# Kernel tuning notes

Measured on AMD Instinct MI355X. Metric: run time of the kernel, lower is better.

The kernel has to match this reference:

```python
import jax, jax.numpy as jnp
import numpy as np

N_NODES = 50000
N_EDGES = 800000
IN_CH = 64
HID = 128


def setup_inputs() -> dict:
    key = jax.random.key(0)
    ks = jax.random.split(key, 10)
    x = jax.random.normal(ks[0], (N_NODES, IN_CH), dtype=jnp.float32)
    edge_index = jax.random.randint(ks[1], (2, N_EDGES), 0, N_NODES, dtype=jnp.int64)
    def lin(k, fan_in, fan_out):
        bound = 1.0 / np.sqrt(fan_in)
        kw, kb = jax.random.split(k)
        W = jax.random.uniform(kw, (fan_in, fan_out), minval=-bound, maxval=bound, dtype=jnp.float32)
        b = jax.random.uniform(kb, (fan_out,), minval=-bound, maxval=bound, dtype=jnp.float32)
        return W, b
    W1a, b1a = lin(ks[2], 2 * IN_CH, HID)
    W1b, b1b = lin(ks[3], HID, HID)
    W2a, b2a = lin(ks[4], 2 * HID, HID)
    W2b, b2b = lin(ks[5], HID, HID)
    return {"x": x, "edge_index": edge_index,
            "W1a": W1a, "b1a": b1a, "W1b": W1b, "b1b": b1b,
            "W2a": W2a, "b2a": b2a, "W2b": W2b, "b2b": b2b}


def _edge_conv(x, src, dst, Wa, ba, Wb, bb):
    # PyG EdgeConv: message = MLP([x_i, x_j - x_i]), aggr = max at target i (dst)
    xi = x[dst]                                   # [E, C] target feats
    xj = x[src]                                   # [E, C] source feats
    m = jnp.concatenate([xi, xj - xi], axis=-1)   # [E, 2C]
    m = jax.nn.relu(m @ Wa + ba) @ Wb + bb        # [E, H]
    agg = jax.ops.segment_max(m, dst, num_segments=N_NODES)
    # nodes with no incoming edge -> 0 (torch_scatter fill value)
    return jnp.where(jnp.isfinite(agg), agg, 0.0)


def reference(x, edge_index, W1a, b1a, W1b, b1b, W2a, b2a, W2b, b2b):
    src = edge_index[0]
    dst = edge_index[1]
    h = _edge_conv(x, src, dst, W1a, b1a, W1b, b1b)
    h = jax.nn.relu(h)
    h = _edge_conv(h, src, dst, W2a, b2a, W2b, b2b)
    return h
```

## Files before the change

kernel.cpp:

```cpp
#include <hip/hip_runtime.h>
#include <stdint.h>

#define N_NODES 50000
#define N_EDGES 800000
#define HID 128
#define NWG_E (N_EDGES / 128)
#define XQ (NWG_E / 8)
#define XR (NWG_E % 8)
#define SCAN_B 196

#define ENC_NEG_INF 0x007FFFFFu

typedef short short8 __attribute__((ext_vector_type(8)));
typedef float f32x4 __attribute__((ext_vector_type(4)));

__device__ __forceinline__ unsigned enc_f32(float f) {
    unsigned u = __float_as_uint(f);
    return (u & 0x80000000u) ? ~u : (u | 0x80000000u);
}
__device__ __forceinline__ float dec_f32(unsigned e) {
    unsigned u = (e & 0x80000000u) ? (e & 0x7FFFFFFFu) : ~e;
    return __uint_as_float(u);
}
__device__ __forceinline__ unsigned short f2bf(float f) {
    unsigned u = __float_as_uint(f);
    unsigned r = (u + 0x7fffu + ((u >> 16) & 1u)) >> 16;
    return (unsigned short)r;
}
__device__ __forceinline__ float bf2f(unsigned short h) {
    return __uint_as_float(((unsigned)h) << 16);
}


__global__ void fill_u32(unsigned* __restrict__ p, int n, unsigned v) {
    int i = blockIdx.x * blockDim.x + threadIdx.x;
    int stride = gridDim.x * blockDim.x;
    for (; i < n; i += stride) p[i] = v;
}

__global__ void prep_wcat(const float* __restrict__ W, int K, float* __restrict__ WC) {
    int idx = blockIdx.x * 256 + threadIdx.x;
    if (idx >= K * 256) return;
    int k = idx >> 8, c = idx & 255;
    float v;
    if (c < 128) v = W[k * 128 + c] - W[(k + K) * 128 + c];
    else         v = W[(k + K) * 128 + (c - 128)];
    WC[idx] = v;
}

__global__ void prep_wfrag(const float* __restrict__ Wb, unsigned short* __restrict__ Wg) {
    int idx = blockIdx.x * 256 + threadIdx.x;
    int j = idx & 7, lane = (idx >> 3) & 63, nt = (idx >> 9) & 7, kt = idx >> 12;
    int k = 32 * kt + 8 * (lane >> 4) + j;
    int n = 16 * nt + (lane & 15);
    float w = Wb[k * 128 + n];
    unsigned short hi = f2bf(w);
    Wg[idx] = hi;
    Wg[16384 + idx] = f2bf(w - bf2f(hi));
}

__global__ void prep_wfrag256(const float* __restrict__ WC, int K, unsigned short* __restrict__ Wg) {
    int idx = blockIdx.x * 256 + threadIdx.x;
    if (idx >= K * 256) return;
    int j = idx & 7, l = (idx >> 3) & 63, nt = (idx >> 9) & 15, kt = idx >> 13;
    int k = 32 * kt + 8 * (l >> 4) + j;
    int n = 16 * nt + (l & 15);
    float v = WC[k * 256 + n];
    unsigned short hi = f2bf(v);
    Wg[idx] = hi;
    Wg[K * 256 + idx] = f2bf(v - bf2f(hi));
}

__global__ void out_decode(unsigned* __restrict__ p, const float* __restrict__ bias, int n) {
    int i = blockIdx.x * blockDim.x + threadIdx.x;
    int stride = gridDim.x * blockDim.x;
    for (; i < n; i += stride) {
        unsigned e = p[i];
        float f = (e == ENC_NEG_INF) ? 0.0f : dec_f32(e) + bias[i & 127];
        ((float*)p)[i] = f;
    }
}


__global__ void hist_dst(const int* __restrict__ dst, unsigned* __restrict__ count) {
    int i = blockIdx.x * blockDim.x + threadIdx.x;
    if (i < N_EDGES) atomicAdd(&count[dst[i]], 1u);
}

__global__ __launch_bounds__(256) void scan_p1(const unsigned* __restrict__ count,
                                               unsigned* __restrict__ bsum) {
    __shared__ unsigned s[256];
    int t = threadIdx.x;
    int i = blockIdx.x * 256 + t;
    s[t] = (i < N_NODES) ? count[i] : 0u;
    __syncthreads();
    for (int off = 128; off > 0; off >>= 1) {
        if (t < off) s[t] += s[t + off];
        __syncthreads();
    }
    if (t == 0) bsum[blockIdx.x] = s[0];
}

__global__ __launch_bounds__(256) void scan_p2(unsigned* __restrict__ bsum) {
    __shared__ unsigned s[256];
    int t = threadIdx.x;
    unsigned v = (t < SCAN_B) ? bsum[t] : 0u;
    s[t] = v;
    __syncthreads();
    for (int off = 1; off < 256; off <<= 1) {
        unsigned x = (t >= off) ? s[t - off] : 0u;
        __syncthreads();
        s[t] += x;
        __syncthreads();
    }
    if (t < SCAN_B) bsum[t] = s[t] - v;
}

__global__ __launch_bounds__(256) void scan_p3(const unsigned* __restrict__ count,
                                               const unsigned* __restrict__ bsum,
                                               unsigned* __restrict__ cursor) {
    __shared__ unsigned s[256];
    int t = threadIdx.x;
    int i = blockIdx.x * 256 + t;
    unsigned v = (i < N_NODES) ? count[i] : 0u;
    s[t] = v;
    __syncthreads();
    for (int off = 1; off < 256; off <<= 1) {
        unsigned x = (t >= off) ? s[t - off] : 0u;
        __syncthreads();
        s[t] += x;
        __syncthreads();
    }
    if (i < N_NODES) cursor[i] = bsum[blockIdx.x] + s[t] - v;
}

__global__ void scatter_edges(const int* __restrict__ src, const int* __restrict__ dst,
                              unsigned* __restrict__ cursor,
                              int* __restrict__ ssrc, int* __restrict__ sdst) {
    int i = blockIdx.x * blockDim.x + threadIdx.x;
    if (i < N_EDGES) {
        int d = dst[i];
        unsigned p = atomicAdd(&cursor[d], 1u);
        ssrc[p] = src[i];
        sdst[p] = d;
    }
}

template<int DEC, int KT>
__global__ __launch_bounds__(256, 2) void gemm_uv_mfma(
        const void* __restrict__ A_,
        const unsigned short* __restrict__ Wg,
        const float* __restrict__ bprev,
        const float* __restrict__ bu,
        unsigned short* __restrict__ C,
        int M) {
    __shared__ char lds[KT * 8192];
    const int K = 32 * KT;
    int tid = threadIdx.x;
    int bx = blockIdx.x, by = blockIdx.y;
    int r0 = bx * 128;
    int w = tid >> 6, l = tid & 63;
    int q = l >> 4, m = l & 15;

    short8 ahi[2][KT];
#pragma unroll
    for (int mt = 0; mt < 2; ++mt) {
        int row = r0 + 32 * w + 16 * mt + m;
        bool ok = row < M;
#pragma unroll
        for (int kt = 0; kt < KT; ++kt) {
            float av[8] = {0.f, 0.f, 0.f, 0.f, 0.f, 0.f, 0.f, 0.f};
            if (ok) {
                if (DEC) {
                    const unsigned* Ar = (const unsigned*)A_ + (size_t)row * K + 32 * kt + 8 * q;
                    uint4 x0 = *(const uint4*)Ar;
                    uint4 x1 = *(const uint4*)(Ar + 4);
                    float4 g0 = *(const float4*)&bprev[32 * kt + 8 * q];
                    float4 g1 = *(const float4*)&bprev[32 * kt + 8 * q + 4];
                    av[0] = fmaxf(dec_f32(x0.x) + g0.x, 0.f);
                    av[1] = fmaxf(dec_f32(x0.y) + g0.y, 0.f);
                    av[2] = fmaxf(dec_f32(x0.z) + g0.z, 0.f);
                    av[3] = fmaxf(dec_f32(x0.w) + g0.w, 0.f);
                    av[4] = fmaxf(dec_f32(x1.x) + g1.x, 0.f);
                    av[5] = fmaxf(dec_f32(x1.y) + g1.y, 0.f);
                    av[6] = fmaxf(dec_f32(x1.z) + g1.z, 0.f);
                    av[7] = fmaxf(dec_f32(x1.w) + g1.w, 0.f);
                } else {
                    const float* Ar = (const float*)A_ + (size_t)row * K + 32 * kt + 8 * q;
                    float4 f0 = *(const float4*)Ar;
                    float4 f1 = *(const float4*)(Ar + 4);
                    av[0] = f0.x; av[1] = f0.y; av[2] = f0.z; av[3] = f0.w;
                    av[4] = f1.x; av[5] = f1.y; av[6] = f1.z; av[7] = f1.w;
                }
            }
            short8 hi;
#pragma unroll
            for (int j = 0; j < 8; ++j) hi[j] = (short)f2bf(av[j]);
            ahi[mt][kt] = hi;
        }
    }

    f32x4 acc[2][8];
#pragma unroll
    for (int mt = 0; mt < 2; ++mt)
#pragma unroll
        for (int nt = 0; nt < 8; ++nt)
            acc[mt][nt] = (f32x4){0.f, 0.f, 0.f, 0.f};

    const short8* bfr = (const short8*)lds;

#pragma unroll
    for (int pl = 0; pl < 2; ++pl) {
        if (pl) __syncthreads();
        {
            const float4* s4 = (const float4*)Wg + (size_t)pl * (K * 32);
            float4* d4 = (float4*)lds;
#pragma unroll
            for (int it = 0; it < 2 * KT; ++it) {
                int f = 256 * it + tid;
                int tl = f >> 6, fin = f & 63;
                int tg = (tl >> 3) * 16 + 8 * by + (tl & 7);
                d4[f] = s4[tg * 64 + fin];
            }
        }
        __syncthreads();
#pragma unroll
        for (int nt = 0; nt < 8; ++nt)
#pragma unroll
            for (int kt = 0; kt < KT; ++kt) {
                short8 b = bfr[(kt * 8 + nt) * 64 + l];
                acc[0][nt] = __builtin_amdgcn_mfma_f32_16x16x32_bf16(ahi[0][kt], b, acc[0][nt], 0, 0, 0);
                acc[1][nt] = __builtin_amdgcn_mfma_f32_16x16x32_bf16(ahi[1][kt], b, acc[1][nt], 0, 0, 0);
            }
    }

#pragma unroll
    for (int nt = 0; nt < 8; ++nt) {
        float bias = (by == 0) ? bu[16 * nt + m] : 0.f;
#pragma unroll
        for (int mt = 0; mt < 2; ++mt) {
            int rowb = r0 + 32 * w + 16 * mt + 4 * q;
#pragma unroll
            for (int r = 0; r < 4; ++r) {
                int row = rowb + r;
                if (row < M)
                    C[(size_t)row * 256 + 128 * by + 16 * nt + m] = f2bf(acc[mt][nt][r] + bias);
            }
        }
    }
}

__global__ __launch_bounds__(256, 4) void edge_mlp_mfma(
        const unsigned short* __restrict__ UV,
        const unsigned short* __restrict__ Wg,
        const int* __restrict__ ssrc,
        const int* __restrict__ sdst,
        unsigned* __restrict__ AGG) {
    __shared__ char lds[33792];
    __shared__ int sdst_s[128];
    int tid = threadIdx.x;
    int orig = blockIdx.x;
    int xcd = orig & 7, ii = orig >> 3;
    int wg = (xcd < XR) ? xcd * (XQ + 1) + ii : XR * (XQ + 1) + (xcd - XR) * XQ + ii;
    int e0 = wg * 128;
    int w = tid >> 6, l = tid & 63;
    int q = l >> 4, m = l & 15;

    if (tid < 128) sdst_s[tid] = sdst[e0 + tid];

    {
        const float4* s4 = (const float4*)Wg;
        float4* d4 = (float4*)lds;
#pragma unroll
        for (int i = 0; i < 8; ++i) d4[tid + 256 * i] = s4[tid + 256 * i];
    }

    short8 ahi[2][4];
#pragma unroll
    for (int mt = 0; mt < 2; ++mt) {
        int e = e0 + 32 * w + 16 * mt + m;
        int d = sdst[e], s = ssrc[e];
        const short8* Ud = (const short8*)&UV[(size_t)d * 256];
        const short8* Vs = (const short8*)&UV[(size_t)s * 256 + 128];
#pragma unroll
        for (int kt = 0; kt < 4; ++kt) {
            short8 u8 = Ud[4 * kt + q];
            short8 v8 = Vs[4 * kt + q];
            short8 hi;
#pragma unroll
            for (int j = 0; j < 8; ++j) {
                float t = bf2f((unsigned short)u8[j]) + bf2f((unsigned short)v8[j]);
                hi[j] = (short)f2bf(fmaxf(t, 0.f));
            }
            ahi[mt][kt] = hi;
        }
    }

    f32x4 acc[2][8];
#pragma unroll
    for (int mt = 0; mt < 2; ++mt)
#pragma unroll
        for (int nt = 0; nt < 8; ++nt)
            acc[mt][nt] = (f32x4){0.f, 0.f, 0.f, 0.f};

    const short8* bfr = (const short8*)lds;

    __syncthreads();
#pragma unroll
    for (int nt = 0; nt < 8; ++nt)
#pragma unroll
        for (int kt = 0; kt < 4; ++kt) {
            short8 b = bfr[(kt * 8 + nt) * 64 + l];
            acc[0][nt] = __builtin_amdgcn_mfma_f32_16x16x32_bf16(ahi[0][kt], b, acc[0][nt], 0, 0, 0);
            acc[1][nt] = __builtin_amdgcn_mfma_f32_16x16x32_bf16(ahi[1][kt], b, acc[1][nt], 0, 0, 0);
        }
    __syncthreads();

    float* M2 = (float*)lds;
#pragma unroll
    for (int ch = 0; ch < 2; ++ch) {
#pragma unroll
        for (int nt = 0; nt < 4; ++nt) {
            int nn = 4 * ch + nt;
#pragma unroll
            for (int mt = 0; mt < 2; ++mt)
#pragma unroll
                for (int r = 0; r < 4; ++r)
                    M2[(32 * w + 16 * mt + 4 * q + r) * 66 + 16 * nt + m] = acc[mt][nn][r];
        }
        __syncthreads();
        {
            int c = tid & 63, h = tid >> 6;
            int eb = 32 * h;
            int cur = sdst_s[eb];
            float mx = -3.402823466e38f;
            for (int e = eb; e < eb + 32; ++e) {
                int de = sdst_s[e];
                if (de != cur) {
                    atomicMax(&AGG[(size_t)cur * 128 + 64 * ch + c], enc_f32(mx));
                    cur = de;
                    mx = -3.402823466e38f;
                }
                mx = fmaxf(mx, M2[e * 66 + c]);
            }
            atomicMax(&AGG[(size_t)cur * 128 + 64 * ch + c], enc_f32(mx));
        }
        __syncthreads();
    }
}


extern "C" void kernel_launch(void* const* d_in, const int* in_sizes, int n_in,
                              void* d_out, int out_size, void* d_ws, size_t ws_size,
                              hipStream_t stream) {
    const float* x   = (const float*)d_in[0];
    const int*   ei  = (const int*)d_in[1];
    const float* W1a = (const float*)d_in[2];
    const float* b1a = (const float*)d_in[3];
    const float* W1b = (const float*)d_in[4];
    const float* b1b = (const float*)d_in[5];
    const float* W2a = (const float*)d_in[6];
    const float* b2a = (const float*)d_in[7];
    const float* W2b = (const float*)d_in[8];
    const float* b2b = (const float*)d_in[9];
    const int* src = ei;
    const int* dst = ei + N_EDGES;

    char* ws = (char*)d_ws;
    unsigned short* UV    = (unsigned short*)ws;
    unsigned*       AGG1  = (unsigned*)(ws + 25600000);
    int*            ssrc  = (int*)(ws + 51200000);
    int*            sdst  = (int*)(ws + 54400000);
    unsigned*       count = (unsigned*)(ws + 57600000);
    unsigned*       cursor= (unsigned*)(ws + 57800000);
    unsigned short* Wg1   = (unsigned short*)(ws + 58000000);
    unsigned short* Wg2   = (unsigned short*)(ws + 58065536);
    float*          WC1   = (float*)(ws + 58131072);
    float*          WC2   = (float*)(ws + 58196608);
    unsigned short* WCg1  = (unsigned short*)(ws + 58327680);
    unsigned short* WCg2  = (unsigned short*)(ws + 58393216);
    unsigned*       bsum  = (unsigned*)(ws + 58655744);

    const int NH = N_NODES * HID;

    prep_wcat<<<64, 256, 0, stream>>>(W1a, 64, WC1);
    prep_wcat<<<128, 256, 0, stream>>>(W2a, 128, WC2);
    prep_wfrag<<<64, 256, 0, stream>>>(W1b, Wg1);
    prep_wfrag<<<64, 256, 0, stream>>>(W2b, Wg2);
    prep_wfrag256<<<64, 256, 0, stream>>>(WC1, 64, WCg1);
    prep_wfrag256<<<128, 256, 0, stream>>>(WC2, 128, WCg2);
    fill_u32<<<2048, 256, 0, stream>>>(AGG1, NH, ENC_NEG_INF);
    fill_u32<<<2048, 256, 0, stream>>>((unsigned*)d_out, NH, ENC_NEG_INF);
    fill_u32<<<196, 256, 0, stream>>>(count, N_NODES, 0u);

    hist_dst<<<3125, 256, 0, stream>>>(dst, count);
    scan_p1<<<SCAN_B, 256, 0, stream>>>(count, bsum);
    scan_p2<<<1, 256, 0, stream>>>(bsum);
    scan_p3<<<SCAN_B, 256, 0, stream>>>(count, bsum, cursor);
    scatter_edges<<<3125, 256, 0, stream>>>(src, dst, cursor, ssrc, sdst);

    gemm_uv_mfma<0, 2><<<dim3(391, 2), 256, 0, stream>>>(x, WCg1, nullptr, b1a, UV, N_NODES);
    edge_mlp_mfma<<<NWG_E, 256, 0, stream>>>(UV, Wg1, ssrc, sdst, AGG1);

    gemm_uv_mfma<1, 4><<<dim3(391, 2), 256, 0, stream>>>(AGG1, WCg2, b1b, b2a, UV, N_NODES);
    edge_mlp_mfma<<<NWG_E, 256, 0, stream>>>(UV, Wg2, ssrc, sdst, (unsigned*)d_out);
    out_decode<<<2048, 256, 0, stream>>>((unsigned*)d_out, b2b, NH);
}
```

Measured before the change: 315.5 us.

## Split edge MLP second layer into two column halves to halve LDS and registers

The second-layer weight fragments are now staged into LDS one 64-column half at a time. The accumulators shrink from 8 to 4 tiles, and the max-reduction runs in 32-column chunks over 16-edge segments. This halves LDS use (34KB to 17KB) and accumulator registers so launch bounds can rise to 5 waves per SIMD. In exchange it adds extra barriers, reloads weights twice per block, and issues more atomicMax calls because segments are shorter. The gathers are also restructured to issue all loads up front, and the prep kernel drops the unused low-part weight split.

```diff
diff --git a/kernel.cpp b/kernel.cpp
--- a/kernel.cpp
+++ b/kernel.cpp
@@ -50,13 +50,12 @@
 
 __global__ void prep_wfrag(const float* __restrict__ Wb, unsigned short* __restrict__ Wg) {
     int idx = blockIdx.x * 256 + threadIdx.x;
-    int j = idx & 7, lane = (idx >> 3) & 63, nt = (idx >> 9) & 7, kt = idx >> 12;
-    int k = 32 * kt + 8 * (lane >> 4) + j;
-    int n = 16 * nt + (lane & 15);
-    float w = Wb[k * 128 + n];
-    unsigned short hi = f2bf(w);
-    Wg[idx] = hi;
-    Wg[16384 + idx] = f2bf(w - bf2f(hi));
+    int j = idx & 7, l = (idx >> 3) & 63, t = idx >> 9;
+    int h = t >> 4, kt = (t >> 2) & 3, ntl = t & 3;
+    int nt = 4 * h + ntl;
+    int k = 32 * kt + 8 * (l >> 4) + j;
+    int n = 16 * nt + (l & 15);
+    Wg[idx] = f2bf(Wb[k * 128 + n]);
 }
 
 __global__ void prep_wfrag256(const float* __restrict__ WC, int K, unsigned short* __restrict__ Wg) {
@@ -250,13 +249,13 @@
     }
 }
 
-__global__ __launch_bounds__(256, 4) void edge_mlp_mfma(
+__global__ __launch_bounds__(256, 5) void edge_mlp_mfma(
         const unsigned short* __restrict__ UV,
         const unsigned short* __restrict__ Wg,
         const int* __restrict__ ssrc,
         const int* __restrict__ sdst,
         unsigned* __restrict__ AGG) {
-    __shared__ char lds[33792];
+    __shared__ char lds[17408];
     __shared__ int sdst_s[128];
     int tid = threadIdx.x;
     int orig = blockIdx.x;
@@ -268,84 +267,91 @@
 
     if (tid < 128) sdst_s[tid] = sdst[e0 + tid];
 
+    short8 ahi[2][4];
     {
-        const float4* s4 = (const float4*)Wg;
-        float4* d4 = (float4*)lds;
-#pragma unroll
-        for (int i = 0; i < 8; ++i) d4[tid + 256 * i] = s4[tid + 256 * i];
-    }
-
-    short8 ahi[2][4];
-#pragma unroll
-    for (int mt = 0; mt < 2; ++mt) {
-        int e = e0 + 32 * w + 16 * mt + m;
-        int d = sdst[e], s = ssrc[e];
-        const short8* Ud = (const short8*)&UV[(size_t)d * 256];
-        const short8* Vs = (const short8*)&UV[(size_t)s * 256 + 128];
-#pragma unroll
-        for (int kt = 0; kt < 4; ++kt) {
-            short8 u8 = Ud[4 * kt + q];
-            short8 v8 = Vs[4 * kt + q];
-            short8 hi;
-#pragma unroll
-            for (int j = 0; j < 8; ++j) {
-                float t = bf2f((unsigned short)u8[j]) + bf2f((unsigned short)v8[j]);
-                hi[j] = (short)f2bf(fmaxf(t, 0.f));
-            }
-            ahi[mt][kt] = hi;
-        }
-    }
-
-    f32x4 acc[2][8];
-#pragma unroll
-    for (int mt = 0; mt < 2; ++mt)
-#pragma unroll
-        for (int nt = 0; nt < 8; ++nt)
-            acc[mt][nt] = (f32x4){0.f, 0.f, 0.f, 0.f};
+        int eA = e0 + 32 * w + m;
+        int d0 = sdst[eA], s0 = ssrc[eA];
+        int d1 = sdst[eA + 16], s1 = ssrc[eA + 16];
+#pragma unroll
+        for (int mt = 0; mt < 2; ++mt) {
+            int d = mt ? d1 : d0, s = mt ? s1 : s0;
+            const short8* Ud = (const short8*)&UV[(size_t)d * 256];
+            const short8* Vs = (const short8*)&UV[(size_t)s * 256 + 128];
+            short8 u0 = Ud[q],      u1 = Ud[4 + q],  u2 = Ud[8 + q],  u3 = Ud[12 + q];
+            short8 v0 = Vs[q],      v1 = Vs[4 + q],  v2 = Vs[8 + q],  v3 = Vs[12 + q];
+            short8 ub[4] = {u0, u1, u2, u3};
+            short8 vb[4] = {v0, v1, v2, v3};
+#pragma unroll
+            for (int kt = 0; kt < 4; ++kt) {
+                short8 hi;
+#pragma unroll
+                for (int j = 0; j < 8; ++j) {
+                    float t = bf2f((unsigned short)ub[kt][j]) + bf2f((unsigned short)vb[kt][j]);
+                    hi[j] = (short)f2bf(fmaxf(t, 0.f));
+                }
+                ahi[mt][kt] = hi;
+            }
+        }
+    }
 
     const short8* bfr = (const short8*)lds;
-
-    __syncthreads();
-#pragma unroll
-    for (int nt = 0; nt < 8; ++nt)
-#pragma unroll
-        for (int kt = 0; kt < 4; ++kt) {
-            short8 b = bfr[(kt * 8 + nt) * 64 + l];
-            acc[0][nt] = __builtin_amdgcn_mfma_f32_16x16x32_bf16(ahi[0][kt], b, acc[0][nt], 0, 0, 0);
-            acc[1][nt] = __builtin_amdgcn_mfma_f32_16x16x32_bf16(ahi[1][kt], b, acc[1][nt], 0, 0, 0);
-        }
-    __syncthreads();
-
     float* M2 = (float*)lds;
-#pragma unroll
-    for (int ch = 0; ch < 2; ++ch) {
-#pragma unroll
-        for (int nt = 0; nt < 4; ++nt) {
-            int nn = 4 * ch + nt;
-#pragma unroll
-            for (int mt = 0; mt < 2; ++mt)
-#pragma unroll
-                for (int r = 0; r < 4; ++r)
-                    M2[(32 * w + 16 * mt + 4 * q + r) * 66 + 16 * nt + m] = acc[mt][nn][r];
-        }
+    f32x4 acc[2][4];
+
+#pragma unroll
+    for (int h = 0; h < 2; ++h) {
         __syncthreads();
         {
-            int c = tid & 63, h = tid >> 6;
-            int eb = 32 * h;
-            int cur = sdst_s[eb];
-            float mx = -3.402823466e38f;
-            for (int e = eb; e < eb + 32; ++e) {
-                int de = sdst_s[e];
-                if (de != cur) {
-                    atomicMax(&AGG[(size_t)cur * 128 + 64 * ch + c], enc_f32(mx));
-                    cur = de;
-                    mx = -3.402823466e38f;
+            const float4* s4 = (const float4*)Wg + h * 1024;
+            float4* d4 = (float4*)lds;
+#pragma unroll
+            for (int i = 0; i < 4; ++i) d4[tid + 256 * i] = s4[tid + 256 * i];
+        }
+        __syncthreads();
+#pragma unroll
+        for (int mt = 0; mt < 2; ++mt)
+#pragma unroll
+            for (int ntl = 0; ntl < 4; ++ntl)
+                acc[mt][ntl] = (f32x4){0.f, 0.f, 0.f, 0.f};
+#pragma unroll
+        for (int ntl = 0; ntl < 4; ++ntl)
+#pragma unroll
+            for (int kt = 0; kt < 4; ++kt) {
+                short8 b = bfr[(kt * 4 + ntl) * 64 + l];
+                acc[0][ntl] = __builtin_amdgcn_mfma_f32_16x16x32_bf16(ahi[0][kt], b, acc[0][ntl], 0, 0, 0);
+                acc[1][ntl] = __builtin_amdgcn_mfma_f32_16x16x32_bf16(ahi[1][kt], b, acc[1][ntl], 0, 0, 0);
+            }
+
+#pragma unroll
+        for (int cn = 0; cn < 2; ++cn) {
+            __syncthreads();
+#pragma unroll
+            for (int nt2 = 0; nt2 < 2; ++nt2) {
+                int ntl = 2 * cn + nt2;
+#pragma unroll
+                for (int mt = 0; mt < 2; ++mt)
+#pragma unroll
+                    for (int r = 0; r < 4; ++r)
+                        M2[(32 * w + 16 * mt + 4 * q + r) * 34 + 16 * nt2 + m] = acc[mt][ntl][r];
+            }
+            __syncthreads();
+            {
+                int c = tid & 31, g = tid >> 5;
+                int eb = 16 * g;
+                int cur = sdst_s[eb];
+                float mx = -3.402823466e38f;
+                for (int e2 = eb; e2 < eb + 16; ++e2) {
+                    int de = sdst_s[e2];
+                    if (de != cur) {
+                        atomicMax(&AGG[(size_t)cur * 128 + 64 * h + 32 * cn + c], enc_f32(mx));
+                        cur = de;
+                        mx = -3.402823466e38f;
+                    }
+                    mx = fmaxf(mx, M2[e2 * 34 + c]);
                 }
-                mx = fmaxf(mx, M2[e * 66 + c]);
-            }
-            atomicMax(&AGG[(size_t)cur * 128 + 64 * ch + c], enc_f32(mx));
-        }
-        __syncthreads();
+                atomicMax(&AGG[(size_t)cur * 128 + 64 * h + 32 * cn + c], enc_f32(mx));
+            }
+        }
     }
 }
 
```

After: 317.8 us. About the same (+0.7%).
